# Optimization experiments

Hardware: AMD Instinct MI355X
Metric: run time of the kernel (lower is better)

Reference implementation:

```python
import jax, jax.numpy as jnp
import numpy as np

B = 1048576
IN_DIM, M, N = 3, 3, 16
C = 2            # num_per_level
W = 1000         # level_dim
MAX_FREQ = 10.0
A_CUBIC = -0.75  # torch grid_sample bicubic coefficient


def setup_inputs() -> dict:
    key = jax.random.key(0)
    k1, k2, k3, k4 = jax.random.split(key, 4)
    x = jax.random.normal(k1, (B, IN_DIM), dtype=jnp.float32)
    # stacked ParameterList of grids: each (1, C, 1, W) -> [N, C, W]
    grids = 0.1 * jax.random.normal(k2, (N, C, W), dtype=jnp.float32)
    G = jax.random.normal(k3, (IN_DIM, M, N), dtype=jnp.float32) * MAX_FREQ
    H = jax.random.normal(k4, (M, N), dtype=jnp.float32) * MAX_FREQ
    return {"x": x, "grids": grids, "G": G, "H": H, "size": 1}


def _cubic_inner(s):
    # weight for |s| <= 1
    return ((A_CUBIC + 2.0) * s - (A_CUBIC + 3.0)) * s * s + 1.0


def _cubic_outer(s):
    # weight for 1 < |s| < 2
    return ((A_CUBIC * s - 5.0 * A_CUBIC) * s + 8.0 * A_CUBIC) * s - 4.0 * A_CUBIC


def reference(x, grids, G, H, size):
    b = x.shape[0]
    in_dim, m, n = G.shape
    w = grids.shape[-1]
    # sin-feature projection: gx[b, i] in [-1, 1]
    a = (x @ G.reshape(in_dim, m * n)).reshape(b, m, n)
    gx = jnp.prod(jnp.sin(a + H.reshape(1, m, n)), axis=1)  # [B, N]
    # grid_sample, mode='bicubic', align_corners=False, padding_mode='zeros'.
    # y coordinate is 0 on an H=1 grid -> ty = 0 -> y-weights are [0,1,0,0],
    # so the 2D bicubic reduces exactly to 1D cubic along W with zero padding.
    ix = ((gx + 1.0) * w - 1.0) / 2.0  # unnormalize (align_corners=False)
    x0 = jnp.floor(ix)
    t = ix - x0
    base = x0.astype(jnp.int32)
    wts = (_cubic_outer(t + 1.0), _cubic_inner(t), _cubic_inner(1.0 - t), _cubic_outer(2.0 - t))
    lvl = jnp.arange(n)[None, :]  # [1, N] -> broadcasts against [B, N] indices
    out = jnp.zeros((b, n, grids.shape[1]), dtype=x.dtype)
    for k in range(4):  # 4 cubic taps (fixed small loop)
        idx = base + (k - 1)
        valid = (idx >= 0) & (idx < w)  # zeros padding for OOB taps
        idxc = jnp.clip(idx, 0, w - 1)
        vals = grids[lvl, :, idxc]  # [B, N, C] gather
        out = out + vals * (wts[k] * valid)[..., None]
    # per-level emb is [B, C]; concat over levels -> [B, N*C]
    return out.reshape(b, -1)
```

## Files before the change

kernel.cpp:

```cpp
#include <hip/hip_runtime.h>


constexpr int B_TOT = 1048576;
constexpr float A_C = -0.75f;

#define BLK 1024
#define WPAD 1004
#define RSTRIDE (WPAD * 2)

__device__ __forceinline__ float hw_sin(float a) {
    float rev = a * 0.15915494309189535f;
    rev = __builtin_amdgcn_fractf(rev);
    return __builtin_amdgcn_sinf(rev);
}

__global__ __launch_bounds__(BLK, 8)
void trig_hashgrid(const float* __restrict__ x, const float* __restrict__ grids,
                   const float* __restrict__ G, const float* __restrict__ H,
                   float* __restrict__ out)
{
    __shared__ float lds[8 * RSTRIDE];
    const int tid  = threadIdx.x;
    const int half = blockIdx.x & 1;
    const int blk  = blockIdx.x >> 1;

    if (tid < 64) {
        int nl = tid >> 3, j = tid & 7;
        int off = (j < 4) ? j : (RSTRIDE - 8 + j);
        lds[nl * RSTRIDE + off] = 0.0f;
    }
    {
        int row = tid >> 7;
        int j   = tid & 127;
        const float* gsrc = grids + half * 16000 + row * 2000;
        float* ldst = lds + row * RSTRIDE;
#pragma unroll
        for (int c = 0; c < 2; ++c)
            for (int w = j; w < 1000; w += 128)
                ldst[(w + 2) * 2 + c] = gsrc[c * 1000 + w];
    }

    const int n_loc = tid & 7;
    const int n     = half * 8 + n_loc;
    const int g     = tid >> 3;

    float G0[3], G1[3], G2[3], Hr[3];
#pragma unroll
    for (int m = 0; m < 3; ++m) {
        G0[m] = G[0 * 48 + m * 16 + n];
        G1[m] = G[1 * 48 + m * 16 + n];
        G2[m] = G[2 * 48 + m * 16 + n];
        Hr[m] = H[m * 16 + n];
    }
    __syncthreads();

    float2* __restrict__ out2 = (float2*)out;
    const float* lrow = &lds[n_loc * RSTRIDE];

#pragma unroll 2
    for (int b = blk * 128 + g; b < B_TOT; b += 512 * 128) {
        float x0 = x[b * 3 + 0];
        float x1 = x[b * 3 + 1];
        float x2 = x[b * 3 + 2];

        float p = 1.0f;
#pragma unroll
        for (int m = 0; m < 3; ++m) {
            float a = fmaf(x0, G0[m], fmaf(x1, G1[m], fmaf(x2, G2[m], Hr[m])));
            p *= hw_sin(a);
        }

        float ix = fmaf(p, 500.0f, 499.5f);
        float xf = floorf(ix);
        float t  = ix - xf;
        int base = (int)xf;
        base = min(max(base, -1), 999);

        float u   = 1.0f - t;
        float tu  = t * u;
        float atu = A_C * tu;
        float w0  = atu * u;
        float w3  = atu * t;
        float w1  = fmaf(fmaf(A_C + 2.0f, t, -(A_C + 3.0f)), t * t, 1.0f);
        float w2  = 1.0f - w0 - w1 - w3;

        const float* tap = lrow + (base + 1) * 2;
        float2 v0 = *(const float2*)(tap + 0);
        float2 v1 = *(const float2*)(tap + 2);
        float2 v2 = *(const float2*)(tap + 4);
        float2 v3 = *(const float2*)(tap + 6);

        float o0 = v0.x * w0, o1 = v0.y * w0;
        o0 = fmaf(v1.x, w1, o0); o1 = fmaf(v1.y, w1, o1);
        o0 = fmaf(v2.x, w2, o0); o1 = fmaf(v2.y, w2, o1);
        o0 = fmaf(v3.x, w3, o0); o1 = fmaf(v3.y, w3, o1);

        out2[b * 16 + n] = make_float2(o0, o1);
    }
}

extern "C" void kernel_launch(void* const* d_in, const int* in_sizes, int n_in,
                              void* d_out, int out_size, void* d_ws, size_t ws_size,
                              hipStream_t stream) {
    const float* x     = (const float*)d_in[0];
    const float* grids = (const float*)d_in[1];
    const float* G     = (const float*)d_in[2];
    const float* H     = (const float*)d_in[3];
    float* out = (float*)d_out;
    trig_hashgrid<<<1024, BLK, 0, stream>>>(x, grids, G, H, out);
}
```

Baseline: 185.4 us.

## Store grid table as half2 in LDS and prefetch next x row

Converts the per-level grid table held in shared memory from fp32 pairs to packed half2, halving LDS footprint and tap-load width, and converts taps back to float before the cubic blend. Also restructures the batch loop into a fixed 16-iteration loop that loads the next row's x coordinates one iteration ahead, hiding global load latency behind the sin/interp math. The fp16 storage loses precision on grid values, which may exceed tolerance.

```diff
diff --git a/kernel.cpp b/kernel.cpp
--- a/kernel.cpp
+++ b/kernel.cpp
@@ -1,4 +1,5 @@
 #include <hip/hip_runtime.h>
+#include <hip/hip_fp16.h>
 
 
 constexpr int B_TOT = 1048576;
@@ -6,7 +7,6 @@
 
 #define BLK 1024
 #define WPAD 1004
-#define RSTRIDE (WPAD * 2)
 
 __device__ __forceinline__ float hw_sin(float a) {
     float rev = a * 0.15915494309189535f;
@@ -19,25 +19,23 @@
                    const float* __restrict__ G, const float* __restrict__ H,
                    float* __restrict__ out)
 {
-    __shared__ float lds[8 * RSTRIDE];
+    __shared__ __half2 lds[8 * WPAD];
     const int tid  = threadIdx.x;
     const int half = blockIdx.x & 1;
     const int blk  = blockIdx.x >> 1;
 
-    if (tid < 64) {
-        int nl = tid >> 3, j = tid & 7;
-        int off = (j < 4) ? j : (RSTRIDE - 8 + j);
-        lds[nl * RSTRIDE + off] = 0.0f;
+    if (tid < 32) {
+        int nl = tid >> 2, j = tid & 3;
+        int off = (j < 2) ? j : (WPAD - 4 + j);
+        lds[nl * WPAD + off] = __floats2half2_rn(0.0f, 0.0f);
     }
     {
         int row = tid >> 7;
         int j   = tid & 127;
         const float* gsrc = grids + half * 16000 + row * 2000;
-        float* ldst = lds + row * RSTRIDE;
-#pragma unroll
-        for (int c = 0; c < 2; ++c)
-            for (int w = j; w < 1000; w += 128)
-                ldst[(w + 2) * 2 + c] = gsrc[c * 1000 + w];
+        __half2* ldst = lds + row * WPAD;
+        for (int w = j; w < 1000; w += 128)
+            ldst[w + 2] = __floats2half2_rn(gsrc[w], gsrc[1000 + w]);
     }
 
     const int n_loc = tid & 7;
@@ -55,13 +53,20 @@
     __syncthreads();
 
     float2* __restrict__ out2 = (float2*)out;
-    const float* lrow = &lds[n_loc * RSTRIDE];
+    const __half2* lrow = &lds[n_loc * WPAD];
+
+    int b = blk * 128 + g;
+    float x0 = x[b * 3 + 0];
+    float x1 = x[b * 3 + 1];
+    float x2 = x[b * 3 + 2];
 
 #pragma unroll 2
-    for (int b = blk * 128 + g; b < B_TOT; b += 512 * 128) {
-        float x0 = x[b * 3 + 0];
-        float x1 = x[b * 3 + 1];
-        float x2 = x[b * 3 + 2];
+    for (int i = 0; i < 16; ++i) {
+        const int bn = b + 512 * 128;
+        const int bs = (i < 15) ? bn : b;
+        float y0 = x[bs * 3 + 0];
+        float y1 = x[bs * 3 + 1];
+        float y2 = x[bs * 3 + 2];
 
         float p = 1.0f;
 #pragma unroll
@@ -84,11 +89,11 @@
         float w1  = fmaf(fmaf(A_C + 2.0f, t, -(A_C + 3.0f)), t * t, 1.0f);
         float w2  = 1.0f - w0 - w1 - w3;
 
-        const float* tap = lrow + (base + 1) * 2;
-        float2 v0 = *(const float2*)(tap + 0);
-        float2 v1 = *(const float2*)(tap + 2);
-        float2 v2 = *(const float2*)(tap + 4);
-        float2 v3 = *(const float2*)(tap + 6);
+        const __half2* tap = lrow + (base + 1);
+        float2 v0 = __half22float2(tap[0]);
+        float2 v1 = __half22float2(tap[1]);
+        float2 v2 = __half22float2(tap[2]);
+        float2 v3 = __half22float2(tap[3]);
 
         float o0 = v0.x * w0, o1 = v0.y * w0;
         o0 = fmaf(v1.x, w1, o0); o1 = fmaf(v1.y, w1, o1);
@@ -96,6 +101,8 @@
         o0 = fmaf(v3.x, w3, o0); o1 = fmaf(v3.y, w3, o1);
 
         out2[b * 16 + n] = make_float2(o0, o1);
+
+        b = bn; x0 = y0; x1 = y1; x2 = y2;
     }
 }
 
```

New measurement: 183.9 us. Within noise of the previous version (-0.8%).
